# Kernel tuning notes

Measured on AMD Instinct MI355X. Metric: run time of the kernel, lower is better.

Reference implementation:

```python
import jax, jax.numpy as jnp
import numpy as np

ENCODER_DIM = 2048
DECODER_DIM = 512
ATTENTION_DIM = 512
BATCH = 512
NUM_PIXELS = 196


def setup_inputs() -> dict:
    key = jax.random.key(0)
    k = jax.random.split(key, 8)
    s_e = 1.0 / np.sqrt(ENCODER_DIM)
    s_d = 1.0 / np.sqrt(DECODER_DIM)
    s_a = 1.0 / np.sqrt(ATTENTION_DIM)
    return {
        "encoder_out": jax.random.normal(k[0], (BATCH, NUM_PIXELS, ENCODER_DIM), jnp.float32),
        "decoder_hidden": jax.random.normal(k[1], (BATCH, DECODER_DIM), jnp.float32),
        "W_enc": jax.random.uniform(k[2], (ENCODER_DIM, ATTENTION_DIM), jnp.float32, -s_e, s_e),
        "b_enc": jax.random.uniform(k[3], (ATTENTION_DIM,), jnp.float32, -s_e, s_e),
        "W_dec": jax.random.uniform(k[4], (DECODER_DIM, ATTENTION_DIM), jnp.float32, -s_d, s_d),
        "b_dec": jax.random.uniform(k[5], (ATTENTION_DIM,), jnp.float32, -s_d, s_d),
        "W_full": jax.random.uniform(k[6], (ATTENTION_DIM,), jnp.float32, -s_a, s_a),
        "b_full": jax.random.uniform(k[7], (), jnp.float32, -s_a, s_a),
    }


def reference(encoder_out, decoder_hidden, W_enc, b_enc, W_dec, b_dec, W_full, b_full):
    # att1: [B, P, A], att2: [B, A]
    att1 = jnp.einsum('bpe,ea->bpa', encoder_out, W_enc) + b_enc
    att2 = decoder_hidden @ W_dec + b_dec
    # scores: [B, P]
    scores = jnp.einsum('bpa,a->bp', jnp.tanh(att1 + att2[:, None, :]), W_full) + b_full
    alpha = jax.nn.softmax(scores, axis=1)
    context = jnp.einsum('bpe,bp->be', encoder_out, alpha)
    return context, alpha
```

## Files before the change

kernel.cpp:

```cpp
#include <hip/hip_runtime.h>
#include <hip/hip_bf16.h>
#include <stdint.h>

#define BATCH 512
#define PIX   196
#define EDIM  2048
#define DDIM  512
#define ADIM  512
#define MROWS (BATCH*PIX)

#define BM 128
#define BN 128
#define BK 32
#define NT (EDIM/BK)

typedef __attribute__((ext_vector_type(8))) short bf16x8;
typedef __attribute__((ext_vector_type(8))) float f32x8;
typedef __attribute__((ext_vector_type(8))) __bf16 bf16v8;
typedef __attribute__((ext_vector_type(4))) float f32x4;

#define GLL16(g, lptr) __builtin_amdgcn_global_load_lds( \
    (const __attribute__((address_space(1))) void*)(g),  \
    (__attribute__((address_space(3))) void*)(lptr), 16, 0, 0)

static __device__ __forceinline__ unsigned short f2bf(float f) {
  union { float f; uint32_t u; } v; v.f = f;
  uint32_t u = v.u;
  return (unsigned short)((u + 0x7FFFu + ((u >> 16) & 1u)) >> 16);
}

static __device__ __forceinline__ bf16x8 cvt8(float4 a, float4 b) {
  f32x8 v = {a.x, a.y, a.z, a.w, b.x, b.y, b.z, b.w};
  bf16v8 c = __builtin_convertvector(v, bf16v8);
  bf16x8 r;
  __builtin_memcpy(&r, &c, 16);
  return r;
}

__global__ void k_transpose_wenc(const float* __restrict__ W,
                                 unsigned short* __restrict__ Bt) {
  __shared__ float tile[32][33];
  const int kt = blockIdx.x;
  const int nt = blockIdx.y;
  const int tx = threadIdx.x, ty = threadIdx.y;
#pragma unroll
  for (int j = 0; j < 4; j++)
    tile[ty + 8*j][tx] = W[(size_t)(kt*32 + ty + 8*j)*ADIM + nt*32 + tx];
  __syncthreads();
#pragma unroll
  for (int j = 0; j < 4; j++)
    Bt[(size_t)(nt*32 + ty + 8*j)*EDIM + kt*32 + tx] = f2bf(tile[tx][ty + 8*j]);
}

__global__ void k_att2(const float* __restrict__ H, const float* __restrict__ Wd,
                       const float* __restrict__ bd, float* __restrict__ att2) {
  __shared__ float h[DDIM];
  const int b = blockIdx.x;
  const int t = threadIdx.x;
  h[t]       = H[(size_t)b*DDIM + t];
  h[t + 256] = H[(size_t)b*DDIM + t + 256];
  __syncthreads();
  float a0 = 0.f, a1 = 0.f;
#pragma unroll 8
  for (int k = 0; k < DDIM; k++) {
    const float hv = h[k];
    a0 += hv * Wd[(size_t)k*ADIM + t];
    a1 += hv * Wd[(size_t)k*ADIM + t + 256];
  }
  att2[(size_t)b*ADIM + t]       = a0 + bd[t];
  att2[(size_t)b*ADIM + t + 256] = a1 + bd[t + 256];
}

__global__ __launch_bounds__(256, 3) void k_gemm_scores(
    const float* __restrict__ enc,
    const unsigned short* __restrict__ Bt,
    const float* __restrict__ b_enc,
    const float* __restrict__ att2,
    const float* __restrict__ W_full,
    float* __restrict__ scores)
{
  __shared__ __align__(16) char ldsA[2*8192];
  __shared__ __align__(16) char ldsB[3*8192];

  const int t   = threadIdx.x;
  const int l   = t & 63;
  const int wid = t >> 6;
  const int wr  = wid >> 1;
  const int wc  = wid & 1;

  const int orig = blockIdx.x;
  const int tile = (orig & 7) * 392 + (orig >> 3);
  const int bm0 = (tile >> 2) * BM;
  const int bn0 = (tile & 3) * BN;

  const int arow = t >> 1;
  const float* srcA = enc + (size_t)(bm0 + arow) * EDIM + (t & 1) * 16;
  const int g0  = (t & 1) * 2;
  const int wA0 = arow*64 + (((g0    ) ^ (arow & 3)) * 16);
  const int wA1 = arow*64 + (((g0 + 1) ^ (arow & 3)) * 16);

  const unsigned short* srcB[2];
#pragma unroll
  for (int j = 0; j < 2; j++) {
    const int idx = j*256 + t;
    const int row = idx >> 2;
    srcB[j] = Bt + (size_t)(bn0 + row) * EDIM + ((idx & 3) ^ (row & 3)) * 8;
  }
  const int dB = wid * 1024;

  const int l15 = l & 15, hi = l >> 4;
  const int ck  = (hi ^ (l15 & 3)) * 16;
  const int baseA = wr*4096 + l15*64 + ck;
  const int baseB = wc*4096 + l15*64 + ck;

  float4 ar[2][4];
  f32x4 acc[4][4] = {};

#define A_ISSUE(SLOT, KT) do {                                   \
    const float* _s = srcA + (size_t)(KT) * BK;                  \
    ar[SLOT][0] = *(const float4*)(_s);                          \
    ar[SLOT][1] = *(const float4*)(_s + 4);                      \
    ar[SLOT][2] = *(const float4*)(_s + 8);                      \
    ar[SLOT][3] = *(const float4*)(_s + 12);                     \
  } while (0)

#define B_GLL(BUF, KT) do {                                      \
    GLL16(srcB[0] + (size_t)(KT)*BK, ldsB + (BUF)*8192 + 0*4096 + dB); \
    GLL16(srcB[1] + (size_t)(KT)*BK, ldsB + (BUF)*8192 + 1*4096 + dB); \
  } while (0)

#define A_WRITE(LBUF, SLOT) do {                                 \
    bf16x8 w0 = cvt8(ar[SLOT][0], ar[SLOT][1]);                  \
    bf16x8 w1 = cvt8(ar[SLOT][2], ar[SLOT][3]);                  \
    *(bf16x8*)(ldsA + (LBUF)*8192 + wA0) = w0;                   \
    *(bf16x8*)(ldsA + (LBUF)*8192 + wA1) = w1;                   \
  } while (0)

#define COMPUTE(BA, BB) do {                                     \
    bf16x8 af[4], bfr[4];                                        \
    _Pragma("unroll")                                            \
    for (int ni = 0; ni < 4; ni++)                               \
      bfr[ni] = *(const bf16x8*)(ldsB + (BB)*8192 + ni*1024 + baseB); \
    _Pragma("unroll")                                            \
    for (int mi = 0; mi < 4; mi++)                               \
      af[mi] = *(const bf16x8*)(ldsA + (BA)*8192 + mi*1024 + baseA); \
    _Pragma("unroll")                                            \
    for (int mi = 0; mi < 4; mi++)                               \
      _Pragma("unroll")                                          \
      for (int ni = 0; ni < 4; ni++)                             \
        acc[mi][ni] = __builtin_amdgcn_mfma_f32_16x16x32_bf16(   \
            af[mi], bfr[ni], acc[mi][ni], 0, 0, 0);              \
  } while (0)

#define TILE(T, CUR, BB, BBS) do {                               \
    A_ISSUE(CUR, (T)+2);                                         \
    B_GLL(BBS, (T)+2);                                           \
    COMPUTE(CUR, BB);                                            \
    asm volatile("s_waitcnt vmcnt(6)" ::: "memory");             \
    A_WRITE((CUR)^1, (CUR)^1);                                   \
    asm volatile("s_waitcnt lgkmcnt(0)" ::: "memory");           \
    __builtin_amdgcn_s_barrier();                                \
  } while (0)

  A_ISSUE(0, 0);
  B_GLL(0, 0);
  A_ISSUE(1, 1);
  B_GLL(1, 1);
  asm volatile("s_waitcnt vmcnt(8)" ::: "memory");
  A_WRITE(0, 0);
  asm volatile("s_waitcnt vmcnt(6) lgkmcnt(0)" ::: "memory");
  __builtin_amdgcn_s_barrier();

  for (int kb = 0; kb < 60; kb += 6) {
    TILE(kb+0, 0, 0, 2);
    TILE(kb+1, 1, 1, 0);
    TILE(kb+2, 0, 2, 1);
    TILE(kb+3, 1, 0, 2);
    TILE(kb+4, 0, 1, 0);
    TILE(kb+5, 1, 2, 1);
  }
  TILE(60, 0, 0, 2);
  TILE(61, 1, 1, 0);
  {
    COMPUTE(0, 2);
    asm volatile("s_waitcnt vmcnt(2)" ::: "memory");
    A_WRITE(1, 1);
    asm volatile("s_waitcnt vmcnt(0) lgkmcnt(0)" ::: "memory");
    __builtin_amdgcn_s_barrier();
  }
  COMPUTE(1, 0);

  float be[4], wf[4];
  int colv[4];
#pragma unroll
  for (int ni = 0; ni < 4; ni++) {
    colv[ni] = bn0 + wc*64 + ni*16 + l15;
    be[ni] = b_enc[colv[ni]];
    wf[ni] = W_full[colv[ni]];
  }
#pragma unroll
  for (int mi = 0; mi < 4; mi++) {
#pragma unroll
    for (int e = 0; e < 4; e++) {
      const int row_l = wr*64 + mi*16 + hi*4 + e;
      const unsigned gr = (unsigned)(bm0 + row_l);
      const unsigned b  = gr / 196u;
      float s = 0.f;
#pragma unroll
      for (int ni = 0; ni < 4; ni++) {
        const float v = acc[mi][ni][e] + be[ni] + att2[(size_t)b*ADIM + colv[ni]];
        s += tanhf(v) * wf[ni];
      }
      s += __shfl_xor(s, 1); s += __shfl_xor(s, 2);
      s += __shfl_xor(s, 4); s += __shfl_xor(s, 8);
      if (l15 == 0) atomicAdd(&scores[gr], s);
    }
  }
}

__global__ void k_softmax(float* __restrict__ sa) {
  __shared__ float red[256];
  const int b = blockIdx.x, t = threadIdx.x;
  const float v = (t < PIX) ? sa[(size_t)b*PIX + t] : -1e30f;
  red[t] = v; __syncthreads();
  for (int s2 = 128; s2 > 0; s2 >>= 1) {
    if (t < s2) red[t] = fmaxf(red[t], red[t + s2]);
    __syncthreads();
  }
  const float m = red[0]; __syncthreads();
  const float e = (t < PIX) ? __expf(v - m) : 0.f;
  red[t] = e; __syncthreads();
  for (int s2 = 128; s2 > 0; s2 >>= 1) {
    if (t < s2) red[t] += red[t + s2];
    __syncthreads();
  }
  const float inv = 1.f / red[0];
  if (t < PIX) sa[(size_t)b*PIX + t] = e * inv;
}

__global__ __launch_bounds__(512) void k_context(
    const float* __restrict__ enc, const float* __restrict__ alpha,
    float* __restrict__ ctx) {
  __shared__ float al[PIX];
  const int b = blockIdx.x, t = threadIdx.x;
  if (t < PIX) al[t] = alpha[(size_t)b*PIX + t];
  __syncthreads();
  const float4* e4 = (const float4*)(enc + (size_t)b * PIX * EDIM);
  float4 acc = {0.f, 0.f, 0.f, 0.f};
#pragma unroll 4
  for (int p = 0; p < PIX; p++) {
    const float4 v = e4[(size_t)p * (EDIM/4) + t];
    const float a = al[p];
    acc.x += v.x * a; acc.y += v.y * a; acc.z += v.z * a; acc.w += v.w * a;
  }
  ((float4*)(ctx + (size_t)b * EDIM))[t] = acc;
}

extern "C" void kernel_launch(void* const* d_in, const int* in_sizes, int n_in,
                              void* d_out, int out_size, void* d_ws, size_t ws_size,
                              hipStream_t stream) {
  (void)in_sizes; (void)n_in; (void)out_size; (void)ws_size;
  const float* enc   = (const float*)d_in[0];
  const float* hid   = (const float*)d_in[1];
  const float* Wenc  = (const float*)d_in[2];
  const float* benc  = (const float*)d_in[3];
  const float* Wdec  = (const float*)d_in[4];
  const float* bdec  = (const float*)d_in[5];
  const float* Wfull = (const float*)d_in[6];

  unsigned short* Bt = (unsigned short*)d_ws;
  float* att2 = (float*)((char*)d_ws + (size_t)ADIM * EDIM * 2);
  float* ctx   = (float*)d_out;
  float* alpha = (float*)d_out + (size_t)BATCH * EDIM;

  hipMemsetAsync(alpha, 0, (size_t)MROWS * sizeof(float), stream);
  k_transpose_wenc<<<dim3(64, 16), dim3(32, 8), 0, stream>>>(Wenc, Bt);
  k_att2<<<BATCH, 256, 0, stream>>>(hid, Wdec, bdec, att2);
  k_gemm_scores<<<3136, 256, 0, stream>>>(enc, Bt, benc, att2, Wfull, alpha);
  k_softmax<<<BATCH, 256, 0, stream>>>(alpha);
  k_context<<<BATCH, 512, 0, stream>>>(enc, alpha, ctx);
}
```

Before: 675.9 us.

## Pre-convert encoder_out to bf16 once and reuse it for GEMM and context

Adds a pass that converts the whole fp32 encoder_out tensor to bf16 in the workspace. A new GEMM kernel then stages both operands with direct global-to-LDS loads in a simple double-buffered loop, replacing the register-staged fp32 convert path. The context reduction now reads the bf16 copy instead of fp32. This removes per-tile conversion work and halves the bytes the two consumers read, but it adds a full read and write of a very large tensor, lowers context precision, and needs a big workspace; otherwise it falls back to the old path.

```diff
diff --git a/kernel.cpp b/kernel.cpp
--- a/kernel.cpp
+++ b/kernel.cpp
@@ -27,6 +27,11 @@
   union { float f; uint32_t u; } v; v.f = f;
   uint32_t u = v.u;
   return (unsigned short)((u + 0x7FFFu + ((u >> 16) & 1u)) >> 16);
+}
+
+static __device__ __forceinline__ float bf2f(unsigned short u) {
+  union { uint32_t u; float f; } v; v.u = ((uint32_t)u) << 16;
+  return v.f;
 }
 
 static __device__ __forceinline__ bf16x8 cvt8(float4 a, float4 b) {
@@ -71,8 +76,20 @@
   att2[(size_t)b*ADIM + t + 256] = a1 + bd[t + 256];
 }
 
-__global__ __launch_bounds__(256, 3) void k_gemm_scores(
-    const float* __restrict__ enc,
+__global__ __launch_bounds__(256) void k_preconvert(const float* __restrict__ in,
+                                                    unsigned short* __restrict__ out,
+                                                    long n8) {
+  long i = (long)blockIdx.x * 256 + threadIdx.x;
+  const long stride = (long)gridDim.x * 256;
+  for (; i < n8; i += stride) {
+    const float4* p = (const float4*)(in + i*8);
+    const float4 a = p[0], b = p[1];
+    *(bf16x8*)(out + i*8) = cvt8(a, b);
+  }
+}
+
+__global__ __launch_bounds__(256, 3) void k_gemm_bf16(
+    const unsigned short* __restrict__ At,
     const unsigned short* __restrict__ Bt,
     const float* __restrict__ b_enc,
     const float* __restrict__ att2,
@@ -80,7 +97,7 @@
     float* __restrict__ scores)
 {
   __shared__ __align__(16) char ldsA[2*8192];
-  __shared__ __align__(16) char ldsB[3*8192];
+  __shared__ __align__(16) char ldsB[2*8192];
 
   const int t   = threadIdx.x;
   const int l   = t & 63;
@@ -93,57 +110,36 @@
   const int bm0 = (tile >> 2) * BM;
   const int bn0 = (tile & 3) * BN;
 
-  const int arow = t >> 1;
-  const float* srcA = enc + (size_t)(bm0 + arow) * EDIM + (t & 1) * 16;
-  const int g0  = (t & 1) * 2;
-  const int wA0 = arow*64 + (((g0    ) ^ (arow & 3)) * 16);
-  const int wA1 = arow*64 + (((g0 + 1) ^ (arow & 3)) * 16);
-
-  const unsigned short* srcB[2];
-#pragma unroll
-  for (int j = 0; j < 2; j++) {
-    const int idx = j*256 + t;
-    const int row = idx >> 2;
-    srcB[j] = Bt + (size_t)(bn0 + row) * EDIM + ((idx & 3) ^ (row & 3)) * 8;
-  }
-  const int dB = wid * 1024;
+  const int r0 = t >> 2, c0 = t & 3;
+  const unsigned short* srcA0 = At + (size_t)(bm0 + r0      ) * EDIM + ((c0 ^ (r0 & 3)) * 8);
+  const unsigned short* srcA1 = At + (size_t)(bm0 + r0 + 64 ) * EDIM + ((c0 ^ (r0 & 3)) * 8);
+  const unsigned short* srcB0 = Bt + (size_t)(bn0 + r0      ) * EDIM + ((c0 ^ (r0 & 3)) * 8);
+  const unsigned short* srcB1 = Bt + (size_t)(bn0 + r0 + 64 ) * EDIM + ((c0 ^ (r0 & 3)) * 8);
+  const int d0 = wid * 1024;
+  const int d1 = 4096 + wid * 1024;
 
   const int l15 = l & 15, hi = l >> 4;
   const int ck  = (hi ^ (l15 & 3)) * 16;
   const int baseA = wr*4096 + l15*64 + ck;
   const int baseB = wc*4096 + l15*64 + ck;
 
-  float4 ar[2][4];
   f32x4 acc[4][4] = {};
 
-#define A_ISSUE(SLOT, KT) do {                                   \
-    const float* _s = srcA + (size_t)(KT) * BK;                  \
-    ar[SLOT][0] = *(const float4*)(_s);                          \
-    ar[SLOT][1] = *(const float4*)(_s + 4);                      \
-    ar[SLOT][2] = *(const float4*)(_s + 8);                      \
-    ar[SLOT][3] = *(const float4*)(_s + 12);                     \
+#define STG(BUF, KT) do {                                        \
+    GLL16(srcA0 + (size_t)(KT)*BK, ldsA + (BUF)*8192 + d0);      \
+    GLL16(srcA1 + (size_t)(KT)*BK, ldsA + (BUF)*8192 + d1);      \
+    GLL16(srcB0 + (size_t)(KT)*BK, ldsB + (BUF)*8192 + d0);      \
+    GLL16(srcB1 + (size_t)(KT)*BK, ldsB + (BUF)*8192 + d1);      \
   } while (0)
 
-#define B_GLL(BUF, KT) do {                                      \
-    GLL16(srcB[0] + (size_t)(KT)*BK, ldsB + (BUF)*8192 + 0*4096 + dB); \
-    GLL16(srcB[1] + (size_t)(KT)*BK, ldsB + (BUF)*8192 + 1*4096 + dB); \
-  } while (0)
-
-#define A_WRITE(LBUF, SLOT) do {                                 \
-    bf16x8 w0 = cvt8(ar[SLOT][0], ar[SLOT][1]);                  \
-    bf16x8 w1 = cvt8(ar[SLOT][2], ar[SLOT][3]);                  \
-    *(bf16x8*)(ldsA + (LBUF)*8192 + wA0) = w0;                   \
-    *(bf16x8*)(ldsA + (LBUF)*8192 + wA1) = w1;                   \
-  } while (0)
-
-#define COMPUTE(BA, BB) do {                                     \
+#define CMP(BUF) do {                                            \
     bf16x8 af[4], bfr[4];                                        \
     _Pragma("unroll")                                            \
     for (int ni = 0; ni < 4; ni++)                               \
-      bfr[ni] = *(const bf16x8*)(ldsB + (BB)*8192 + ni*1024 + baseB); \
+      bfr[ni] = *(const bf16x8*)(ldsB + (BUF)*8192 + ni*1024 + baseB); \
     _Pragma("unroll")                                            \
     for (int mi = 0; mi < 4; mi++)                               \
-      af[mi] = *(const bf16x8*)(ldsA + (BA)*8192 + mi*1024 + baseA); \
+      af[mi] = *(const bf16x8*)(ldsA + (BUF)*8192 + mi*1024 + baseA); \
     _Pragma("unroll")                                            \
     for (int mi = 0; mi < 4; mi++)                               \
       _Pragma("unroll")                                          \
@@ -152,43 +148,16 @@
             af[mi], bfr[ni], acc[mi][ni], 0, 0, 0);              \
   } while (0)
 
-#define TILE(T, CUR, BB, BBS) do {                               \
-    A_ISSUE(CUR, (T)+2);                                         \
-    B_GLL(BBS, (T)+2);                                           \
-    COMPUTE(CUR, BB);                                            \
-    asm volatile("s_waitcnt vmcnt(6)" ::: "memory");             \
-    A_WRITE((CUR)^1, (CUR)^1);                                   \
-    asm volatile("s_waitcnt lgkmcnt(0)" ::: "memory");           \
-    __builtin_amdgcn_s_barrier();                                \
-  } while (0)
-
-  A_ISSUE(0, 0);
-  B_GLL(0, 0);
-  A_ISSUE(1, 1);
-  B_GLL(1, 1);
-  asm volatile("s_waitcnt vmcnt(8)" ::: "memory");
-  A_WRITE(0, 0);
-  asm volatile("s_waitcnt vmcnt(6) lgkmcnt(0)" ::: "memory");
-  __builtin_amdgcn_s_barrier();
-
-  for (int kb = 0; kb < 60; kb += 6) {
-    TILE(kb+0, 0, 0, 2);
-    TILE(kb+1, 1, 1, 0);
-    TILE(kb+2, 0, 2, 1);
-    TILE(kb+3, 1, 0, 2);
-    TILE(kb+4, 0, 1, 0);
-    TILE(kb+5, 1, 2, 1);
-  }
-  TILE(60, 0, 0, 2);
-  TILE(61, 1, 1, 0);
-  {
-    COMPUTE(0, 2);
-    asm volatile("s_waitcnt vmcnt(2)" ::: "memory");
-    A_WRITE(1, 1);
-    asm volatile("s_waitcnt vmcnt(0) lgkmcnt(0)" ::: "memory");
-    __builtin_amdgcn_s_barrier();
-  }
-  COMPUTE(1, 0);
+  STG(0, 0);
+  __syncthreads();
+  for (int kt = 0; kt < NT; kt += 2) {
+    STG(1, kt + 1);
+    CMP(0);
+    __syncthreads();
+    if (kt + 2 < NT) STG(0, kt + 2);
+    CMP(1);
+    __syncthreads();
+  }
 
   float be[4], wf[4];
   int colv[4];
@@ -238,6 +207,118 @@
   if (t < PIX) sa[(size_t)b*PIX + t] = e * inv;
 }
 
+__global__ __launch_bounds__(256) void k_context_bf16(
+    const unsigned short* __restrict__ encbf, const float* __restrict__ alpha,
+    float* __restrict__ ctx) {
+  __shared__ float al[PIX];
+  const int b = blockIdx.x, t = threadIdx.x;
+  if (t < PIX) al[t] = alpha[(size_t)b*PIX + t];
+  __syncthreads();
+  const unsigned short* e = encbf + (size_t)b * PIX * EDIM + t * 8;
+  float acc[8] = {};
+  for (int p = 0; p < PIX; p++) {
+    const bf16x8 v = *(const bf16x8*)(e + (size_t)p * EDIM);
+    const float a = al[p];
+#pragma unroll
+    for (int j = 0; j < 8; j++)
+      acc[j] += a * bf2f((unsigned short)v[j]);
+  }
+  float4 o0 = {acc[0], acc[1], acc[2], acc[3]};
+  float4 o1 = {acc[4], acc[5], acc[6], acc[7]};
+  float4* dst = (float4*)(ctx + (size_t)b * EDIM + t * 8);
+  dst[0] = o0; dst[1] = o1;
+}
+
+__global__ __launch_bounds__(256, 3) void k_gemm_scores(
+    const float* __restrict__ enc, const unsigned short* __restrict__ Bt,
+    const float* __restrict__ b_enc, const float* __restrict__ att2,
+    const float* __restrict__ W_full, float* __restrict__ scores) {
+  __shared__ __align__(16) char ldsA[2*8192];
+  __shared__ __align__(16) char ldsB[3*8192];
+  const int t = threadIdx.x, l = t & 63, wid = t >> 6;
+  const int wr = wid >> 1, wc = wid & 1;
+  const int orig = blockIdx.x;
+  const int tile = (orig & 7) * 392 + (orig >> 3);
+  const int bm0 = (tile >> 2) * BM, bn0 = (tile & 3) * BN;
+  const int arow = t >> 1;
+  const float* srcA = enc + (size_t)(bm0 + arow) * EDIM + (t & 1) * 16;
+  const int g0 = (t & 1) * 2;
+  const int wA0 = arow*64 + (((g0    ) ^ (arow & 3)) * 16);
+  const int wA1 = arow*64 + (((g0 + 1) ^ (arow & 3)) * 16);
+  const unsigned short* srcB[2];
+#pragma unroll
+  for (int j = 0; j < 2; j++) {
+    const int idx = j*256 + t; const int row = idx >> 2;
+    srcB[j] = Bt + (size_t)(bn0 + row) * EDIM + ((idx & 3) ^ (row & 3)) * 8;
+  }
+  const int dB = wid * 1024;
+  const int l15 = l & 15, hi = l >> 4;
+  const int ck = (hi ^ (l15 & 3)) * 16;
+  const int baseA = wr*4096 + l15*64 + ck;
+  const int baseB = wc*4096 + l15*64 + ck;
+  float4 ar[2][4];
+  f32x4 acc[4][4] = {};
+#define F_A_ISSUE(SLOT, KT) do { const float* _s = srcA + (size_t)(KT) * BK; \
+    ar[SLOT][0] = *(const float4*)(_s); ar[SLOT][1] = *(const float4*)(_s + 4); \
+    ar[SLOT][2] = *(const float4*)(_s + 8); ar[SLOT][3] = *(const float4*)(_s + 12); } while (0)
+#define F_B_GLL(BUF, KT) do { \
+    GLL16(srcB[0] + (size_t)(KT)*BK, ldsB + (BUF)*8192 + dB); \
+    GLL16(srcB[1] + (size_t)(KT)*BK, ldsB + (BUF)*8192 + 4096 + dB); } while (0)
+#define F_A_WRITE(LBUF, SLOT) do { \
+    bf16x8 w0 = cvt8(ar[SLOT][0], ar[SLOT][1]); bf16x8 w1 = cvt8(ar[SLOT][2], ar[SLOT][3]); \
+    *(bf16x8*)(ldsA + (LBUF)*8192 + wA0) = w0; *(bf16x8*)(ldsA + (LBUF)*8192 + wA1) = w1; } while (0)
+#define F_COMPUTE(BA, BB) do { bf16x8 af[4], bfr[4]; \
+    _Pragma("unroll") for (int ni = 0; ni < 4; ni++) \
+      bfr[ni] = *(const bf16x8*)(ldsB + (BB)*8192 + ni*1024 + baseB); \
+    _Pragma("unroll") for (int mi = 0; mi < 4; mi++) \
+      af[mi] = *(const bf16x8*)(ldsA + (BA)*8192 + mi*1024 + baseA); \
+    _Pragma("unroll") for (int mi = 0; mi < 4; mi++) \
+      _Pragma("unroll") for (int ni = 0; ni < 4; ni++) \
+        acc[mi][ni] = __builtin_amdgcn_mfma_f32_16x16x32_bf16(af[mi], bfr[ni], acc[mi][ni], 0, 0, 0); } while (0)
+#define F_TILE(T, CUR, BB, BBS) do { F_A_ISSUE(CUR, (T)+2); F_B_GLL(BBS, (T)+2); \
+    F_COMPUTE(CUR, BB); asm volatile("s_waitcnt vmcnt(6)" ::: "memory"); \
+    F_A_WRITE((CUR)^1, (CUR)^1); asm volatile("s_waitcnt lgkmcnt(0)" ::: "memory"); \
+    __builtin_amdgcn_s_barrier(); } while (0)
+  F_A_ISSUE(0, 0); F_B_GLL(0, 0); F_A_ISSUE(1, 1); F_B_GLL(1, 1);
+  asm volatile("s_waitcnt vmcnt(8)" ::: "memory");
+  F_A_WRITE(0, 0);
+  asm volatile("s_waitcnt vmcnt(6) lgkmcnt(0)" ::: "memory");
+  __builtin_amdgcn_s_barrier();
+  for (int kb = 0; kb < 60; kb += 6) {
+    F_TILE(kb+0, 0, 0, 2); F_TILE(kb+1, 1, 1, 0); F_TILE(kb+2, 0, 2, 1);
+    F_TILE(kb+3, 1, 0, 2); F_TILE(kb+4, 0, 1, 0); F_TILE(kb+5, 1, 2, 1);
+  }
+  F_TILE(60, 0, 0, 2); F_TILE(61, 1, 1, 0);
+  { F_COMPUTE(0, 2); asm volatile("s_waitcnt vmcnt(2)" ::: "memory");
+    F_A_WRITE(1, 1); asm volatile("s_waitcnt vmcnt(0) lgkmcnt(0)" ::: "memory");
+    __builtin_amdgcn_s_barrier(); }
+  F_COMPUTE(1, 0);
+  float be[4], wf[4]; int colv[4];
+#pragma unroll
+  for (int ni = 0; ni < 4; ni++) {
+    colv[ni] = bn0 + wc*64 + ni*16 + l15;
+    be[ni] = b_enc[colv[ni]]; wf[ni] = W_full[colv[ni]];
+  }
+#pragma unroll
+  for (int mi = 0; mi < 4; mi++) {
+#pragma unroll
+    for (int e = 0; e < 4; e++) {
+      const int row_l = wr*64 + mi*16 + hi*4 + e;
+      const unsigned gr = (unsigned)(bm0 + row_l);
+      const unsigned b  = gr / 196u;
+      float s = 0.f;
+#pragma unroll
+      for (int ni = 0; ni < 4; ni++) {
+        const float v = acc[mi][ni][e] + be[ni] + att2[(size_t)b*ADIM + colv[ni]];
+        s += tanhf(v) * wf[ni];
+      }
+      s += __shfl_xor(s, 1); s += __shfl_xor(s, 2);
+      s += __shfl_xor(s, 4); s += __shfl_xor(s, 8);
+      if (l15 == 0) atomicAdd(&scores[gr], s);
+    }
+  }
+}
+
 __global__ __launch_bounds__(512) void k_context(
     const float* __restrict__ enc, const float* __restrict__ alpha,
     float* __restrict__ ctx) {
@@ -259,7 +340,7 @@
 extern "C" void kernel_launch(void* const* d_in, const int* in_sizes, int n_in,
                               void* d_out, int out_size, void* d_ws, size_t ws_size,
                               hipStream_t stream) {
-  (void)in_sizes; (void)n_in; (void)out_size; (void)ws_size;
+  (void)in_sizes; (void)n_in; (void)out_size;
   const float* enc   = (const float*)d_in[0];
   const float* hid   = (const float*)d_in[1];
   const float* Wenc  = (const float*)d_in[2];
@@ -268,15 +349,34 @@
   const float* bdec  = (const float*)d_in[5];
   const float* Wfull = (const float*)d_in[6];
 
-  unsigned short* Bt = (unsigned short*)d_ws;
-  float* att2 = (float*)((char*)d_ws + (size_t)ADIM * EDIM * 2);
   float* ctx   = (float*)d_out;
   float* alpha = (float*)d_out + (size_t)BATCH * EDIM;
 
-  hipMemsetAsync(alpha, 0, (size_t)MROWS * sizeof(float), stream);
-  k_transpose_wenc<<<dim3(64, 16), dim3(32, 8), 0, stream>>>(Wenc, Bt);
-  k_att2<<<BATCH, 256, 0, stream>>>(hid, Wdec, bdec, att2);
-  k_gemm_scores<<<3136, 256, 0, stream>>>(enc, Bt, benc, att2, Wfull, alpha);
-  k_softmax<<<BATCH, 256, 0, stream>>>(alpha);
-  k_context<<<BATCH, 512, 0, stream>>>(enc, alpha, ctx);
-}
+  const size_t encbf_b = (size_t)MROWS * EDIM * 2;
+  const size_t bt_b    = (size_t)ADIM * EDIM * 2;
+  const size_t att2_b  = (size_t)BATCH * ADIM * 4;
+
+  if (ws_size >= encbf_b + bt_b + att2_b) {
+    unsigned short* encbf = (unsigned short*)d_ws;
+    unsigned short* Bt    = (unsigned short*)((char*)d_ws + encbf_b);
+    float*          att2  = (float*)((char*)d_ws + encbf_b + bt_b);
+
+    hipMemsetAsync(alpha, 0, (size_t)MROWS * sizeof(float), stream);
+    k_transpose_wenc<<<dim3(64, 16), dim3(32, 8), 0, stream>>>(Wenc, Bt);
+    k_att2<<<BATCH, 256, 0, stream>>>(hid, Wdec, bdec, att2);
+    k_preconvert<<<2048, 256, 0, stream>>>(enc, encbf, (long)MROWS * EDIM / 8);
+    k_gemm_bf16<<<3136, 256, 0, stream>>>(encbf, Bt, benc, att2, Wfull, alpha);
+    k_softmax<<<BATCH, 256, 0, stream>>>(alpha);
+    k_context_bf16<<<BATCH, 256, 0, stream>>>(encbf, alpha, ctx);
+  } else {
+    unsigned short* Bt   = (unsigned short*)d_ws;
+    float*          att2 = (float*)((char*)d_ws + bt_b);
+
+    hipMemsetAsync(alpha, 0, (size_t)MROWS * sizeof(float), stream);
+    k_transpose_wenc<<<dim3(64, 16), dim3(32, 8), 0, stream>>>(Wenc, Bt);
+    k_att2<<<BATCH, 256, 0, stream>>>(hid, Wdec, bdec, att2);
+    k_gemm_scores<<<3136, 256, 0, stream>>>(enc, Bt, benc, att2, Wfull, alpha);
+    k_softmax<<<BATCH, 256, 0, stream>>>(alpha);
+    k_context<<<BATCH, 512, 0, stream>>>(enc, alpha, ctx);
+  }
+}
```

Measured after the change: 683.2 us. Within noise of the previous version (+1.1%).
